# Performance work log

Measured on AMD Instinct MI355X. Metric: run time of the kernel, lower is better.

## Reference

```python
import jax, jax.numpy as jnp
import numpy as np
import math


def _rotate_one(kernel, angle):
    """Bilinear-rotate one group kernel [Cg,Cg,kH,kW] by scalar angle."""
    kH, kW = kernel.shape[2], kernel.shape[3]
    cy, cx = (kH - 1) / 2.0, (kW - 1) / 2.0
    y = jnp.arange(kH, dtype=kernel.dtype) - cy
    x = jnp.arange(kW, dtype=kernel.dtype) - cx
    yy, xx = jnp.meshgrid(y, x, indexing='ij')
    c, s = jnp.cos(angle), jnp.sin(angle)
    x_rot = xx * c + yy * s + cx
    y_rot = -xx * s + yy * c + cy
    x0 = jnp.clip(jnp.floor(x_rot), 0, kW - 2)
    y0 = jnp.clip(jnp.floor(y_rot), 0, kH - 2)
    x1 = x0 + 1
    y1 = y0 + 1
    w00 = (x1 - x_rot) * (y1 - y_rot)
    w01 = (x1 - x_rot) * (y_rot - y0)
    w10 = (x_rot - x0) * (y1 - y_rot)
    w11 = (x_rot - x0) * (y_rot - y0)
    x0i = x0.astype(jnp.int32); y0i = y0.astype(jnp.int32)
    x1i = x1.astype(jnp.int32); y1i = y1.astype(jnp.int32)
    # gather over last two dims: [Cg,Cg,kH,kW]
    return (w00 * kernel[..., y0i, x0i] + w01 * kernel[..., y1i, x0i]
            + w10 * kernel[..., y0i, x1i] + w11 * kernel[..., y1i, x1i])


def setup_inputs() -> dict:
    key = jax.random.key(0)
    ks = jax.random.split(key, 6)
    B, C, H, W = 16, 256, 64, 64
    G, Cg, K = 8, 32, 3
    HID = C // 4  # 64
    fan_out = Cg * K * K
    return {
        'x': jax.random.normal(ks[0], (B, C, H, W), jnp.float32),
        'base_kernel': jax.random.normal(ks[1], (G, Cg, Cg, K, K), jnp.float32) * np.sqrt(2.0 / fan_out),
        'ap_w1': jax.random.normal(ks[2], (HID, C), jnp.float32) * np.sqrt(1.0 / C),
        'ap_b1': jnp.zeros((HID,), jnp.float32),
        'ap_w2': jax.random.normal(ks[3], (G, HID), jnp.float32) * np.sqrt(1.0 / HID),
        'ap_b2': jnp.zeros((G,), jnp.float32),
        'meta_w1': jax.random.normal(ks[4], (HID, C), jnp.float32) * np.sqrt(1.0 / C),
        'meta_b1': jnp.zeros((HID,), jnp.float32),
        'meta_w2': jax.random.normal(ks[5], (C, HID), jnp.float32) * np.sqrt(1.0 / HID),
        'meta_b2': jnp.zeros((C,), jnp.float32),
    }


def reference(x, base_kernel, ap_w1, ap_b1, ap_w2, ap_b2,
              meta_w1, meta_b1, meta_w2, meta_b2):
    B, C, H, W = x.shape
    G, Cg = base_kernel.shape[0], base_kernel.shape[1]
    K = base_kernel.shape[-1]
    pad = (K - 1) // 2

    pooled = x.mean(axis=(2, 3))  # [B,C] == AdaptiveAvgPool2d(1) on 1x1-conv MLPs

    # angle predictor: 1x1 conv MLP -> tanh -> scale by pi/4
    h = jax.nn.relu(pooled @ ap_w1.T + ap_b1)
    angles = jnp.tanh(h @ ap_w2.T + ap_b2) * (math.pi / 4)  # [B,G]

    # per-(sample,group) bilinear kernel rotation, fully vectorized
    rot = jax.vmap(jax.vmap(_rotate_one), in_axes=(None, 0))(base_kernel, angles)
    # rot: [B,G,Cg,Cg,K,K] -> per-sample grouped conv via feature_group_count=B*G
    w = rot.reshape(B * C, Cg, K, K)
    out = jax.lax.conv_general_dilated(
        x.reshape(1, B * C, H, W), w, window_strides=(1, 1),
        padding=[(pad, pad), (pad, pad)],
        dimension_numbers=('NCHW', 'OIHW', 'NCHW'),
        feature_group_count=B * G)
    feat = out.reshape(B, C, H, W)

    # meta modulation: squeeze-excite style gate
    m = jax.nn.relu(pooled @ meta_w1.T + meta_b1)
    mod = jax.nn.sigmoid(m @ meta_w2.T + meta_b2)  # [B,C]
    return feat * mod[:, :, None, None]
```

## Files before the change

### kernel.cpp

```cpp
#include <hip/hip_runtime.h>
#include <math.h>

#define B_ 16
#define C_ 256
#define H_ 64
#define W_ 64
#define G_ 8
#define CG_ 32
#define HID_ 64

typedef __attribute__((ext_vector_type(8))) short short8;
typedef __attribute__((ext_vector_type(4))) float floatx4;

__device__ inline unsigned short f2bf(float f) {
    union { float f; unsigned u; } v; v.f = f;
    unsigned r = v.u + 0x7fffu + ((v.u >> 16) & 1u);
    return (unsigned short)(r >> 16);
}

__global__ void pool_kernel(const float* __restrict__ x, float* __restrict__ pooled) {
    int idx = blockIdx.x;
    const float4* src = (const float4*)(x + (size_t)idx * (H_ * W_));
    float s = 0.f;
#pragma unroll
    for (int i = 0; i < 4; ++i) {
        float4 v = src[threadIdx.x + i * 256];
        s += v.x + v.y + v.z + v.w;
    }
#pragma unroll
    for (int off = 32; off > 0; off >>= 1) s += __shfl_down(s, off, 64);
    __shared__ float wsum[4];
    if ((threadIdx.x & 63) == 0) wsum[threadIdx.x >> 6] = s;
    __syncthreads();
    if (threadIdx.x == 0)
        pooled[idx] = (wsum[0] + wsum[1] + wsum[2] + wsum[3]) * (1.0f / 4096.0f);
}

__global__ void mlp_kernel(const float* __restrict__ pooled,
                           const float* __restrict__ ap_w1, const float* __restrict__ ap_b1,
                           const float* __restrict__ ap_w2, const float* __restrict__ ap_b2,
                           const float* __restrict__ mw1, const float* __restrict__ mb1,
                           const float* __restrict__ mw2, const float* __restrict__ mb2,
                           float* __restrict__ angles, float* __restrict__ modg) {
    int b = blockIdx.x, tid = threadIdx.x;
    __shared__ float sp[C_], ha[HID_], hm[HID_];
    sp[tid] = pooled[b * C_ + tid];
    __syncthreads();
    if (tid < 64) {
        const float* wr = ap_w1 + tid * C_;
        float s = ap_b1[tid];
        for (int c = 0; c < C_; ++c) s = fmaf(sp[c], wr[c], s);
        ha[tid] = fmaxf(s, 0.f);
    } else if (tid < 128) {
        int t = tid - 64;
        const float* wr = mw1 + t * C_;
        float s = mb1[t];
        for (int c = 0; c < C_; ++c) s = fmaf(sp[c], wr[c], s);
        hm[t] = fmaxf(s, 0.f);
    }
    __syncthreads();
    if (tid < G_) {
        const float* wr = ap_w2 + tid * HID_;
        float s = ap_b2[tid];
        for (int i = 0; i < HID_; ++i) s = fmaf(ha[i], wr[i], s);
        angles[b * G_ + tid] = tanhf(s) * 0.78539816339744830962f;
    }
    {
        const float* wr = mw2 + tid * HID_;
        float s = mb2[tid];
        for (int i = 0; i < HID_; ++i) s = fmaf(hm[i], wr[i], s);
        modg[b * C_ + tid] = 1.0f / (1.0f + expf(-s));
    }
}

__global__ void rot_kernel(const float* __restrict__ base, const float* __restrict__ angles,
                           unsigned short* __restrict__ rotw) {
    int e = blockIdx.x * 256 + threadIdx.x;
    int ci = e & 31;
    int co = (e >> 5) & 31;
    int t = e >> 10;
    int k = t % 9;
    int bg = t / 9;
    int b = bg >> 3, g = bg & 7;

    float ang = angles[b * G_ + g];
    float cc = cosf(ang), ss = sinf(ang);
    int i = k / 3, j = k % 3;
    float fx = (float)(j - 1), fy = (float)(i - 1);
    float xr = fx * cc + fy * ss + 1.0f;
    float yr = -fx * ss + fy * cc + 1.0f;
    float x0f = fminf(fmaxf(floorf(xr), 0.f), 1.f);
    float y0f = fminf(fmaxf(floorf(yr), 0.f), 1.f);
    float w00 = (x0f + 1.f - xr) * (y0f + 1.f - yr);
    float w01 = (x0f + 1.f - xr) * (yr - y0f);
    float w10 = (xr - x0f) * (y0f + 1.f - yr);
    float w11 = (xr - x0f) * (yr - y0f);
    int x0 = (int)x0f, y0 = (int)y0f;

    const float* bk = base + (((size_t)(g * CG_ + co) * CG_ + ci) * 9);
    float v = w00 * bk[y0 * 3 + x0] + w01 * bk[(y0 + 1) * 3 + x0] +
              w10 * bk[y0 * 3 + x0 + 1] + w11 * bk[(y0 + 1) * 3 + x0 + 1];
    rotw[e] = f2bf(v);
}

__global__ __launch_bounds__(256, 2) void conv_mfma(const float* __restrict__ x,
                                                    const unsigned short* __restrict__ rotw,
                                                    const float* __restrict__ modg,
                                                    float* __restrict__ out) {
    __shared__ __align__(16) unsigned short sW[9 * 32 * 32];
    __shared__ __align__(16) unsigned short sX[10 * 66 * 32];
    __shared__ float smod[32];
    int bg = blockIdx.x;
    int b = bg >> 3, g = bg & 7;
    int r0 = blockIdx.y * 8;
    int tid = threadIdx.x;

    {
        const float4* src = (const float4*)(rotw + (size_t)bg * 9216);
        float4* dst = (float4*)sW;
#pragma unroll
        for (int i = 0; i < 5; ++i) {
            int idx = tid + i * 256;
            if (idx < 1152) dst[idx] = src[idx];
        }
    }
    if (tid < 32) smod[tid] = modg[b * C_ + g * CG_ + tid];

    {
        int ci = tid & 31;
        int cellbase = tid >> 5;
#pragma unroll
        for (int i = 0; i < 20; ++i) {
            int cell = cellbase + i * 8;
            int c4 = cell & 15, r = cell >> 4;
            int grow = r0 - 1 + r;
            float4 v = make_float4(0.f, 0.f, 0.f, 0.f);
            if (grow >= 0 && grow < H_)
                v = *(const float4*)(x + (((size_t)(b * C_ + g * CG_ + ci) * H_ + grow) * W_ + c4 * 4));
            int base = (r * 66 + 1 + c4 * 4) * 32 + ci;
            sX[base] = f2bf(v.x);
            sX[base + 32] = f2bf(v.y);
            sX[base + 64] = f2bf(v.z);
            sX[base + 96] = f2bf(v.w);
        }
#pragma unroll
        for (int i = 0; i < 3; ++i) {
            int idx = tid + i * 256;
            if (idx < 640) {
                int ci2 = idx & 31;
                int t2 = idx >> 5;
                int side = t2 & 1, r = t2 >> 1;
                sX[(r * 66 + side * 65) * 32 + ci2] = 0;
            }
        }
    }
    __syncthreads();

    int lane = tid & 63;
    int wv = tid >> 6;
    int nlo = lane & 15;
    int quad = lane >> 4;

    floatx4 acc0[8], acc1[8];
#pragma unroll
    for (int nt = 0; nt < 8; ++nt) {
        acc0[nt] = (floatx4){0.f, 0.f, 0.f, 0.f};
        acc1[nt] = (floatx4){0.f, 0.f, 0.f, 0.f};
    }

#pragma unroll
    for (int k9 = 0; k9 < 9; ++k9) {
        const int dy = k9 / 3 - 1, dx = k9 % 3 - 1;
        short8 a0 = *(const short8*)&sW[((k9 * 32) + nlo) * 32 + quad * 8];
        short8 a1 = *(const short8*)&sW[((k9 * 32) + 16 + nlo) * 32 + quad * 8];
#pragma unroll
        for (int nt = 0; nt < 8; ++nt) {
            int rr = wv * 2 + (nt >> 2) + 1 + dy;
            int cc = (nt & 3) * 16 + nlo + 1 + dx;
            short8 bf = *(const short8*)&sX[(rr * 66 + cc) * 32 + quad * 8];
            acc0[nt] = __builtin_amdgcn_mfma_f32_16x16x32_bf16(a0, bf, acc0[nt], 0, 0, 0);
            acc1[nt] = __builtin_amdgcn_mfma_f32_16x16x32_bf16(a1, bf, acc1[nt], 0, 0, 0);
        }
    }

    float gm[2][4];
#pragma unroll
    for (int mt = 0; mt < 2; ++mt)
#pragma unroll
        for (int reg = 0; reg < 4; ++reg) gm[mt][reg] = smod[mt * 16 + quad * 4 + reg];

#pragma unroll
    for (int nt = 0; nt < 8; ++nt) {
        int row = r0 + wv * 2 + (nt >> 2);
        int col = (nt & 3) * 16 + nlo;
#pragma unroll
        for (int reg = 0; reg < 4; ++reg) {
            int co0 = quad * 4 + reg;
            out[((size_t)(b * C_ + g * CG_ + co0) * H_ + row) * W_ + col] = acc0[nt][reg] * gm[0][reg];
            int co1 = 16 + quad * 4 + reg;
            out[((size_t)(b * C_ + g * CG_ + co1) * H_ + row) * W_ + col] = acc1[nt][reg] * gm[1][reg];
        }
    }
}

extern "C" void kernel_launch(void* const* d_in, const int* in_sizes, int n_in,
                              void* d_out, int out_size, void* d_ws, size_t ws_size,
                              hipStream_t stream) {
    const float* x      = (const float*)d_in[0];
    const float* basek  = (const float*)d_in[1];
    const float* ap_w1  = (const float*)d_in[2];
    const float* ap_b1  = (const float*)d_in[3];
    const float* ap_w2  = (const float*)d_in[4];
    const float* ap_b2  = (const float*)d_in[5];
    const float* mw1    = (const float*)d_in[6];
    const float* mb1    = (const float*)d_in[7];
    const float* mw2    = (const float*)d_in[8];
    const float* mb2    = (const float*)d_in[9];
    float* out = (float*)d_out;

    float* wsf    = (float*)d_ws;
    float* pooled = wsf;
    float* angles = wsf + 4096;
    float* modg   = wsf + 8192;
    unsigned short* rotw = (unsigned short*)(wsf + 12288);

    pool_kernel<<<B_ * C_, 256, 0, stream>>>(x, pooled);
    mlp_kernel<<<B_, 256, 0, stream>>>(pooled, ap_w1, ap_b1, ap_w2, ap_b2,
                                       mw1, mb1, mw2, mb2, angles, modg);
    rot_kernel<<<(B_ * G_ * CG_ * CG_ * 9) / 256, 256, 0, stream>>>(basek, angles, rotw);
    dim3 cgrid(B_ * G_, H_ / 8);
    conv_mfma<<<cgrid, 256, 0, stream>>>(x, rotw, modg, out);
}
```

Measured before the change: 166.8 us.

## Fuse pooling with bf16 channel-last transpose and stream conv tiles via LDS loads

The pooling kernel is replaced by a pass that reads x once, writes a bf16 channel-interleaved copy (8 channels per 16-byte chunk), and emits per-row partial sums that the MLP reduces. The conv kernel then fills its shared-memory tiles with direct global-to-LDS 16-byte loads instead of loading fp32 and converting with scattered 2-byte LDS stores. The aim is to drop the per-block fp32 conversion and scalar LDS writes and to reuse the conversion across the overlapping row tiles. In exchange it adds an extra bf16 write and read of the whole activation tensor, and the MLP now reduces 64 partial rows per channel. It also vectorises the MLP loops and uses fast sin/cos.

```diff
diff --git a/kernel.cpp b/kernel.cpp
--- a/kernel.cpp
+++ b/kernel.cpp
@@ -18,47 +18,87 @@
     return (unsigned short)(r >> 16);
 }
 
-__global__ void pool_kernel(const float* __restrict__ x, float* __restrict__ pooled) {
-    int idx = blockIdx.x;
-    const float4* src = (const float4*)(x + (size_t)idx * (H_ * W_));
-    float s = 0.f;
-#pragma unroll
-    for (int i = 0; i < 4; ++i) {
-        float4 v = src[threadIdx.x + i * 256];
-        s += v.x + v.y + v.z + v.w;
-    }
-#pragma unroll
-    for (int off = 32; off > 0; off >>= 1) s += __shfl_down(s, off, 64);
-    __shared__ float wsum[4];
-    if ((threadIdx.x & 63) == 0) wsum[threadIdx.x >> 6] = s;
-    __syncthreads();
-    if (threadIdx.x == 0)
-        pooled[idx] = (wsum[0] + wsum[1] + wsum[2] + wsum[3]) * (1.0f / 4096.0f);
-}
-
-__global__ void mlp_kernel(const float* __restrict__ pooled,
+__device__ __forceinline__ void gld16(const unsigned short* g, unsigned short* l) {
+    __builtin_amdgcn_global_load_lds(
+        (const __attribute__((address_space(1))) unsigned int*)g,
+        (__attribute__((address_space(3))) unsigned int*)l, 16, 0, 0);
+}
+
+__global__ void xpose_pool(const float* __restrict__ x,
+                           unsigned short* __restrict__ xT,
+                           float* __restrict__ rowsum) {
+    int bid = blockIdx.x;
+    int tid = threadIdx.x;
+    int w = tid & 63, q = tid >> 6;
+    int h = bid & 63, bg = bid >> 6;
+
+    const float* src = x + (((size_t)bg * 32 + q * 8) * 64 + h) * 64 + w;
+    float v[8];
+#pragma unroll
+    for (int j = 0; j < 8; ++j) v[j] = src[(size_t)j * 4096];
+
+    short8 sv;
+#pragma unroll
+    for (int j = 0; j < 8; ++j) sv[j] = (short)f2bf(v[j]);
+    *(short8*)(xT + ((size_t)(bid * 4 + q) * 64 + w) * 8) = sv;
+
+#pragma unroll
+    for (int j = 0; j < 8; ++j) {
+#pragma unroll
+        for (int off = 32; off > 0; off >>= 1) v[j] += __shfl_down(v[j], off, 64);
+    }
+    if (w == 0) {
+        float* rs = rowsum + (size_t)bid * 32 + q * 8;
+#pragma unroll
+        for (int j = 0; j < 8; ++j) rs[j] = v[j];
+    }
+}
+
+__global__ void mlp_kernel(const float* __restrict__ rowsum,
                            const float* __restrict__ ap_w1, const float* __restrict__ ap_b1,
                            const float* __restrict__ ap_w2, const float* __restrict__ ap_b2,
                            const float* __restrict__ mw1, const float* __restrict__ mb1,
                            const float* __restrict__ mw2, const float* __restrict__ mb2,
                            float* __restrict__ angles, float* __restrict__ modg) {
     int b = blockIdx.x, tid = threadIdx.x;
-    __shared__ float sp[C_], ha[HID_], hm[HID_];
-    sp[tid] = pooled[b * C_ + tid];
+    __shared__ __align__(16) float sp[C_];
+    __shared__ __align__(16) float ha[HID_], hm[HID_];
+
+    {
+        const float* rs = rowsum + ((size_t)(b * 8 + (tid >> 5)) * 64) * 32 + (tid & 31);
+        float s = 0.f;
+#pragma unroll
+        for (int h = 0; h < 64; ++h) s += rs[h * 32];
+        sp[tid] = s * (1.0f / 4096.0f);
+    }
     __syncthreads();
+
     if (tid < 64) {
-        const float* wr = ap_w1 + tid * C_;
+        const float4* wr = (const float4*)(ap_w1 + tid * C_);
+        const float4* p4 = (const float4*)sp;
         float s = ap_b1[tid];
-        for (int c = 0; c < C_; ++c) s = fmaf(sp[c], wr[c], s);
+#pragma unroll
+        for (int i = 0; i < 64; ++i) {
+            float4 wv = wr[i], pv = p4[i];
+            s = fmaf(pv.x, wv.x, s); s = fmaf(pv.y, wv.y, s);
+            s = fmaf(pv.z, wv.z, s); s = fmaf(pv.w, wv.w, s);
+        }
         ha[tid] = fmaxf(s, 0.f);
     } else if (tid < 128) {
         int t = tid - 64;
-        const float* wr = mw1 + t * C_;
+        const float4* wr = (const float4*)(mw1 + t * C_);
+        const float4* p4 = (const float4*)sp;
         float s = mb1[t];
-        for (int c = 0; c < C_; ++c) s = fmaf(sp[c], wr[c], s);
+#pragma unroll
+        for (int i = 0; i < 64; ++i) {
+            float4 wv = wr[i], pv = p4[i];
+            s = fmaf(pv.x, wv.x, s); s = fmaf(pv.y, wv.y, s);
+            s = fmaf(pv.z, wv.z, s); s = fmaf(pv.w, wv.w, s);
+        }
         hm[t] = fmaxf(s, 0.f);
     }
     __syncthreads();
+
     if (tid < G_) {
         const float* wr = ap_w2 + tid * HID_;
         float s = ap_b2[tid];
@@ -84,7 +124,7 @@
     int b = bg >> 3, g = bg & 7;
 
     float ang = angles[b * G_ + g];
-    float cc = cosf(ang), ss = sinf(ang);
+    float cc = __cosf(ang), ss = __sinf(ang);
     int i = k / 3, j = k % 3;
     float fx = (float)(j - 1), fy = (float)(i - 1);
     float xr = fx * cc + fy * ss + 1.0f;
@@ -103,61 +143,46 @@
     rotw[e] = f2bf(v);
 }
 
-__global__ __launch_bounds__(256, 2) void conv_mfma(const float* __restrict__ x,
+__global__ __launch_bounds__(256, 2) void conv_mfma(const unsigned short* __restrict__ xT,
                                                     const unsigned short* __restrict__ rotw,
                                                     const float* __restrict__ modg,
                                                     float* __restrict__ out) {
     __shared__ __align__(16) unsigned short sW[9 * 32 * 32];
-    __shared__ __align__(16) unsigned short sX[10 * 66 * 32];
+    __shared__ __align__(16) unsigned short sX[10 * 4 * 66 * 8];
     __shared__ float smod[32];
     int bg = blockIdx.x;
     int b = bg >> 3, g = bg & 7;
     int r0 = blockIdx.y * 8;
     int tid = threadIdx.x;
-
-    {
-        const float4* src = (const float4*)(rotw + (size_t)bg * 9216);
-        float4* dst = (float4*)sW;
-#pragma unroll
-        for (int i = 0; i < 5; ++i) {
-            int idx = tid + i * 256;
-            if (idx < 1152) dst[idx] = src[idx];
-        }
-    }
-    if (tid < 32) smod[tid] = modg[b * C_ + g * CG_ + tid];
-
-    {
-        int ci = tid & 31;
-        int cellbase = tid >> 5;
-#pragma unroll
-        for (int i = 0; i < 20; ++i) {
-            int cell = cellbase + i * 8;
-            int c4 = cell & 15, r = cell >> 4;
-            int grow = r0 - 1 + r;
-            float4 v = make_float4(0.f, 0.f, 0.f, 0.f);
-            if (grow >= 0 && grow < H_)
-                v = *(const float4*)(x + (((size_t)(b * C_ + g * CG_ + ci) * H_ + grow) * W_ + c4 * 4));
-            int base = (r * 66 + 1 + c4 * 4) * 32 + ci;
-            sX[base] = f2bf(v.x);
-            sX[base + 32] = f2bf(v.y);
-            sX[base + 64] = f2bf(v.z);
-            sX[base + 96] = f2bf(v.w);
-        }
-#pragma unroll
-        for (int i = 0; i < 3; ++i) {
-            int idx = tid + i * 256;
-            if (idx < 640) {
-                int ci2 = idx & 31;
-                int t2 = idx >> 5;
-                int side = t2 & 1, r = t2 >> 1;
-                sX[(r * 66 + side * 65) * 32 + ci2] = 0;
-            }
-        }
-    }
-    __syncthreads();
-
     int lane = tid & 63;
     int wv = tid >> 6;
+
+#pragma unroll
+    for (int i = 0; i < 5; ++i) {
+        int idx = tid + i * 256;
+        if (idx < 1152)
+            gld16(rotw + (size_t)bg * 9216 + idx * 8, &sW[idx * 8]);
+    }
+
+#pragma unroll
+    for (int i = 0; i < 10; ++i) {
+        int s = wv + i * 4;
+        int r = s >> 2, q = s & 3;
+        int grow = r0 - 1 + r;
+        unsigned short* lp = &sX[((size_t)s * 66 + 1 + lane) * 8];
+        if (grow >= 0 && grow < H_) {
+            gld16(xT + ((((size_t)bg * 64 + grow) * 4 + q) * 64 + lane) * 8, lp);
+        } else {
+            *(short8*)lp = (short8){0, 0, 0, 0, 0, 0, 0, 0};
+        }
+    }
+    if (tid < 80) {
+        int s = tid >> 1, side = tid & 1;
+        *(short8*)&sX[((size_t)s * 66 + side * 65) * 8] = (short8){0, 0, 0, 0, 0, 0, 0, 0};
+    }
+    if (tid < 32) smod[tid] = modg[b * C_ + g * CG_ + tid];
+    __syncthreads();
+
     int nlo = lane & 15;
     int quad = lane >> 4;
 
@@ -177,7 +202,7 @@
         for (int nt = 0; nt < 8; ++nt) {
             int rr = wv * 2 + (nt >> 2) + 1 + dy;
             int cc = (nt & 3) * 16 + nlo + 1 + dx;
-            short8 bf = *(const short8*)&sX[(rr * 66 + cc) * 32 + quad * 8];
+            short8 bf = *(const short8*)&sX[(((size_t)rr * 4 + quad) * 66 + cc) * 8];
             acc0[nt] = __builtin_amdgcn_mfma_f32_16x16x32_bf16(a0, bf, acc0[nt], 0, 0, 0);
             acc1[nt] = __builtin_amdgcn_mfma_f32_16x16x32_bf16(a1, bf, acc1[nt], 0, 0, 0);
         }
@@ -219,15 +244,16 @@
     float* out = (float*)d_out;
 
     float* wsf    = (float*)d_ws;
-    float* pooled = wsf;
-    float* angles = wsf + 4096;
-    float* modg   = wsf + 8192;
-    unsigned short* rotw = (unsigned short*)(wsf + 12288);
-
-    pool_kernel<<<B_ * C_, 256, 0, stream>>>(x, pooled);
-    mlp_kernel<<<B_, 256, 0, stream>>>(pooled, ap_w1, ap_b1, ap_w2, ap_b2,
+    float* rowsum = wsf;
+    float* angles = wsf + 262144;
+    float* modg   = wsf + 262272;
+    unsigned short* rotw = (unsigned short*)(wsf + 266368);
+    unsigned short* xT   = (unsigned short*)(wsf + 856192);
+
+    xpose_pool<<<B_ * G_ * H_, 256, 0, stream>>>(x, xT, rowsum);
+    mlp_kernel<<<B_, 256, 0, stream>>>(rowsum, ap_w1, ap_b1, ap_w2, ap_b2,
                                        mw1, mb1, mw2, mb2, angles, modg);
     rot_kernel<<<(B_ * G_ * CG_ * CG_ * 9) / 256, 256, 0, stream>>>(basek, angles, rotw);
     dim3 cgrid(B_ * G_, H_ / 8);
-    conv_mfma<<<cgrid, 256, 0, stream>>>(x, rotw, modg, out);
-}
+    conv_mfma<<<cgrid, 256, 0, stream>>>(xT, rotw, modg, out);
+}
```

Result: faster. 163.5 us (-2.0%).
